# Kernel tuning notes

Measured on AMD Instinct MI355X. Metric: run time of the kernel, lower is better.

The kernel has to match this reference:

```python
import jax, jax.numpy as jnp
import numpy as np

B, LATENT = 8192, 1024
NR, NC = 12, 12                      # nb_rows, nb_cols
H0, W0 = NR + 2, NC + 2              # 14x14 after reshape
EPS = 1e-5
SLOPE = 0.01                         # LeakyReLU default


def setup_inputs() -> dict:
    key = jax.random.key(0)
    ks = jax.random.split(key, 9)
    s = 0.05
    return {
        "x": jax.random.normal(ks[0], (B, LATENT), jnp.float32),
        "fc_w": jax.random.normal(ks[1], (H0 * W0 * 36, LATENT), jnp.float32) * s,
        "fc_b": jax.random.normal(ks[2], (H0 * W0 * 36,), jnp.float32) * s,
        "conv_w": jax.random.normal(ks[3], (16, 36, 2, 2), jnp.float32) * s,
        "conv_b": jax.random.normal(ks[4], (16,), jnp.float32) * s,
        "gamma": jnp.ones((16,), jnp.float32),
        "beta": jnp.zeros((16,), jnp.float32),
        # locally-connected weights: (out_ch, in_ch, Hout, Wout, k*k)
        "lw1": jax.random.normal(ks[5], (6, 16, H0 - 1, W0 - 1, 4), jnp.float32) * s,
        "lw2": jax.random.normal(ks[6], (1, 6, H0 - 2, W0 - 2, 4), jnp.float32) * s,
    }


def _leaky(x):
    return jnp.where(x >= 0, x, SLOPE * x)


def _local_conv2(x, w):
    # x: (B,C,H,W); w: (O,C,Ho,Wo,4) with k=2, stride 1, no padding
    Ho, Wo = w.shape[2], w.shape[3]
    patches = jnp.stack(
        [x[:, :, dy:dy + Ho, dx:dx + Wo] for dy in (0, 1) for dx in (0, 1)],
        axis=-1)  # (B,C,Ho,Wo,4)
    return jnp.einsum('bchwk,ochwk->bohw', patches, w)


def reference(x, fc_w, fc_b, conv_w, conv_b, gamma, beta, lw1, lw2):
    # fc -> view(B, H0, W0, 36) -> permute to NCHW
    h = x @ fc_w.T + fc_b
    h = h.reshape(B, H0, W0, 36).transpose(0, 3, 1, 2)  # (B,36,14,14)
    # Conv2d k=2 padding='same' (torch pads bottom/right for even kernels)
    h = jax.lax.conv_general_dilated(
        h, conv_w, window_strides=(1, 1), padding=((0, 1), (0, 1)),
        dimension_numbers=('NCHW', 'OIHW', 'NCHW')) + conv_b[None, :, None, None]
    h = _leaky(h)
    # BatchNorm2d (training mode: batch stats, biased var)
    mu = h.mean(axis=(0, 2, 3), keepdims=True)
    var = h.var(axis=(0, 2, 3), keepdims=True)
    h = (h - mu) * jax.lax.rsqrt(var + EPS)
    h = h * gamma[None, :, None, None] + beta[None, :, None, None]
    # locally-connected stack: 14x14 -> 13x13 -> 12x12
    h = _leaky(_local_conv2(h, lw1))
    return _local_conv2(h, lw2)  # (B,1,12,12)
```

## Files before the change

kernel.cpp:

```cpp
#include <hip/hip_runtime.h>


#define SLOPE 0.01f

typedef __bf16 bf16x8 __attribute__((ext_vector_type(8)));
typedef float f32x4 __attribute__((ext_vector_type(4)));

typedef const __attribute__((address_space(1))) void* gas_ptr;
typedef __attribute__((address_space(3))) void* las_ptr;

__device__ __forceinline__ void load16_to_lds(const void* g, void* l) {
  __builtin_amdgcn_global_load_lds((gas_ptr)g, (las_ptr)l, 16, 0, 0);
}

__device__ __forceinline__ unsigned short f2bf(float f) {
  union { float f; unsigned int u; } v; v.f = f;
  unsigned int r = v.u + 0x7FFFu + ((v.u >> 16) & 1u);
  return (unsigned short)(r >> 16);
}
__device__ __forceinline__ float bfbits2f(unsigned int bits16) {
  union { unsigned int u; float f; } v; v.u = bits16 << 16;
  return v.f;
}
__device__ __forceinline__ float leaky(float v) { return v >= 0.f ? v : SLOPE * v; }

__global__ void k_cast_x(const float* __restrict__ x, unsigned short* __restrict__ xb,
                         float* __restrict__ stats) {
  if (blockIdx.x == 0 && threadIdx.x < 32) stats[threadIdx.x] = 0.f;
  int gid = blockIdx.x * 256 + threadIdx.x;
  const float4* x4 = (const float4*)x;
  float4 a = x4[gid * 2], b = x4[gid * 2 + 1];
  union { unsigned short s[8]; uint4 v; } o;
  o.s[0] = f2bf(a.x); o.s[1] = f2bf(a.y); o.s[2] = f2bf(a.z); o.s[3] = f2bf(a.w);
  o.s[4] = f2bf(b.x); o.s[5] = f2bf(b.y); o.s[6] = f2bf(b.z); o.s[7] = f2bf(b.w);
  ((uint4*)xb)[gid] = o.v;
}

__global__ void k_fold(const float* __restrict__ fc_w, const float* __restrict__ fc_b,
                       const float* __restrict__ conv_w, const float* __restrict__ conv_b,
                       unsigned short* __restrict__ Wc, float* __restrict__ bc) {
  __shared__ float cw[2304];
  int blk = blockIdx.x, t = threadIdx.x;
  if (blk == 196) {
    uint4 z = make_uint4(0, 0, 0, 0);
    uint4* dst = (uint4*)(Wc + 3136 * 1024);
    for (int i = t; i < 8192; i += 256) dst[i] = z;
    for (int i = 3136 + t; i < 3200; i += 256) bc[i] = 0.f;
    return;
  }
  for (int i = t; i < 2304; i += 256) cw[i] = conv_w[i];
  __syncthreads();
  int i0 = blk / 14, j0 = blk - (blk / 14) * 14;
  float acc[16][4];
#pragma unroll
  for (int o = 0; o < 16; o++)
#pragma unroll
    for (int q = 0; q < 4; q++) acc[o][q] = 0.f;
  for (int c = 0; c < 36; c++) {
#pragma unroll
    for (int dy = 0; dy < 2; dy++) {
      int ii = i0 + dy; if (ii > 13) continue;
#pragma unroll
      for (int dx = 0; dx < 2; dx++) {
        int jj = j0 + dx; if (jj > 13) continue;
        int row = (ii * 14 + jj) * 36 + c;
        float4 f = *(const float4*)(fc_w + row * 1024 + t * 4);
        int kk = dy * 2 + dx;
#pragma unroll
        for (int o = 0; o < 16; o++) {
          float w = cw[(o * 36 + c) * 4 + kk];
          acc[o][0] += w * f.x; acc[o][1] += w * f.y;
          acc[o][2] += w * f.z; acc[o][3] += w * f.w;
        }
      }
    }
  }
#pragma unroll
  for (int o = 0; o < 16; o++) {
    int n = o * 196 + i0 * 14 + j0;
    union { unsigned short s[4]; uint2 v; } u;
    u.s[0] = f2bf(acc[o][0]); u.s[1] = f2bf(acc[o][1]);
    u.s[2] = f2bf(acc[o][2]); u.s[3] = f2bf(acc[o][3]);
    *(uint2*)(Wc + n * 1024 + t * 4) = u.v;
  }
  if (t < 16) {
    int o = t;
    float b = conv_b[o];
    for (int c = 0; c < 36; c++)
      for (int dy = 0; dy < 2; dy++) {
        int ii = i0 + dy; if (ii > 13) continue;
        for (int dx = 0; dx < 2; dx++) {
          int jj = j0 + dx; if (jj > 13) continue;
          b += cw[(o * 36 + c) * 4 + dy * 2 + dx] * fc_b[(ii * 14 + jj) * 36 + c];
        }
      }
    bc[o * 196 + i0 * 14 + j0] = b;
  }
}

__global__ __launch_bounds__(256, 2) void k_gemm(const unsigned short* __restrict__ Xb,
                                                 const unsigned short* __restrict__ Wcb,
                                                 const float* __restrict__ bc,
                                                 unsigned short* __restrict__ h2) {
  __shared__ __align__(16) char lds[16384];
  const int t = threadIdx.x;
  const int w = t >> 6, lane = t & 63;
  const int quad = lane >> 4, l15 = lane & 15;
  const int m0 = blockIdx.y * 128, n0 = blockIdx.x * 128;
  const int mrow = t & 127, tko = t >> 7;
  const unsigned short* ga = Xb + (m0 + mrow) * 1024 + tko * 8;
  const unsigned short* gb = Wcb + (n0 + mrow) * 1024 + tko * 8;
  char* lA = lds;
  char* lB = lds + 8192;
  const int wbase = w * 1024;
  const int wm0 = (w >> 1) * 64, wn0 = (w & 1) * 64;

  f32x4 acc[4][4];
#pragma unroll
  for (int a = 0; a < 4; a++)
#pragma unroll
    for (int b = 0; b < 4; b++) acc[a][b] = (f32x4){0.f, 0.f, 0.f, 0.f};

  for (int kb = 0; kb < 1024; kb += 32) {
    __syncthreads();
    load16_to_lds(ga + kb,      lA + wbase);
    load16_to_lds(ga + kb + 16, lA + 4096 + wbase);
    load16_to_lds(gb + kb,      lB + wbase);
    load16_to_lds(gb + kb + 16, lB + 4096 + wbase);
    __syncthreads();

    bf16x8 af[4], bfr[4];
#pragma unroll
    for (int mb = 0; mb < 4; mb++)
      af[mb] = *(const bf16x8*)(lA + quad * 2048 + (wm0 + mb * 16 + l15) * 16);
#pragma unroll
    for (int nb = 0; nb < 4; nb++)
      bfr[nb] = *(const bf16x8*)(lB + quad * 2048 + (wn0 + nb * 16 + l15) * 16);
#pragma unroll
    for (int mb = 0; mb < 4; mb++)
#pragma unroll
      for (int nb = 0; nb < 4; nb++)
        acc[mb][nb] = __builtin_amdgcn_mfma_f32_16x16x32_bf16(af[mb], bfr[nb], acc[mb][nb], 0, 0, 0);
  }

#pragma unroll
  for (int nb = 0; nb < 4; nb++) {
    int col = n0 + wn0 + nb * 16 + l15;
    float bias = bc[col];
#pragma unroll
    for (int mb = 0; mb < 4; mb++) {
#pragma unroll
      for (int r = 0; r < 4; r++) {
        int row = m0 + wm0 + mb * 16 + quad * 4 + r;
        float v = acc[mb][nb][r] + bias;
        h2[row * 3200 + col] = f2bf(leaky(v));
      }
    }
  }
}

__global__ void k_stats(const unsigned short* __restrict__ h2, float* __restrict__ stats) {
  int o = blockIdx.x;
  int b0 = blockIdx.y * 64;
  float s = 0.f, s2 = 0.f;
  for (int i = threadIdx.x; i < 64 * 98; i += 256) {
    int b = i / 98, q = i - b * 98;
    unsigned int u = *(const unsigned int*)(h2 + (b0 + b) * 3200 + o * 196 + q * 2);
    float v0 = bfbits2f(u & 0xffffu), v1 = bfbits2f(u >> 16);
    s += v0 + v1; s2 += v0 * v0 + v1 * v1;
  }
  for (int off = 32; off; off >>= 1) {
    s += __shfl_down(s, off, 64);
    s2 += __shfl_down(s2, off, 64);
  }
  __shared__ float ps[8];
  int wv = threadIdx.x >> 6, lane = threadIdx.x & 63;
  if (lane == 0) { ps[wv * 2] = s; ps[wv * 2 + 1] = s2; }
  __syncthreads();
  if (threadIdx.x == 0) {
    atomicAdd(&stats[o],      ps[0] + ps[2] + ps[4] + ps[6]);
    atomicAdd(&stats[16 + o], ps[1] + ps[3] + ps[5] + ps[7]);
  }
}

__global__ __launch_bounds__(256) void k_tail(const unsigned short* __restrict__ h2,
                                              const float* __restrict__ stats,
                                              const float* __restrict__ gamma,
                                              const float* __restrict__ beta,
                                              const float* __restrict__ lw1,
                                              const float* __restrict__ lw2,
                                              float* __restrict__ out) {
  __shared__ unsigned short h3[4 * 3138];
  __shared__ float h4[4 * 1015];
  __shared__ float sc[16], sh[16];
  int b0 = blockIdx.x * 4, t = threadIdx.x;
  if (t < 16) {
    const float inv = 1.f / 1605632.f;
    float mean = stats[t] * inv;
    float var = stats[16 + t] * inv - mean * mean;
    float rstd = rsqrtf(var + 1e-5f);
    float s = gamma[t] * rstd;
    sc[t] = s; sh[t] = beta[t] - mean * s;
  }
  __syncthreads();
  for (int i = t; i < 6272; i += 256) {
    int bb = i / 1568, q = i - bb * 1568;
    int n = q * 2, o = n / 196;
    unsigned int u = *(const unsigned int*)(h2 + (b0 + bb) * 3200 + n);
    float v0 = bfbits2f(u & 0xffffu) * sc[o] + sh[o];
    float v1 = bfbits2f(u >> 16) * sc[o] + sh[o];
    unsigned int pk = (unsigned int)f2bf(v0) | ((unsigned int)f2bf(v1) << 16);
    *(unsigned int*)(h3 + bb * 3138 + n) = pk;
  }
  __syncthreads();
  for (int u = t; u < 312; u += 256) {
    int bb = u & 3, rest = u >> 2;
    int o = rest / 13, y = rest - o * 13;
    float acc[13];
#pragma unroll
    for (int x = 0; x < 13; x++) acc[x] = 0.f;
    const unsigned short* hb = h3 + bb * 3138;
    for (int c = 0; c < 16; c++) {
      float r0[14], r1[14];
      const unsigned int* p0 = (const unsigned int*)(hb + c * 196 + y * 14);
      const unsigned int* p1 = (const unsigned int*)(hb + c * 196 + (y + 1) * 14);
#pragma unroll
      for (int q = 0; q < 7; q++) {
        unsigned int v0 = p0[q], v1 = p1[q];
        r0[2 * q] = bfbits2f(v0 & 0xffffu); r0[2 * q + 1] = bfbits2f(v0 >> 16);
        r1[2 * q] = bfbits2f(v1 & 0xffffu); r1[2 * q + 1] = bfbits2f(v1 >> 16);
      }
      const float* wp = lw1 + (((o * 16 + c) * 13 + y) * 13) * 4;
#pragma unroll
      for (int x = 0; x < 13; x++)
        acc[x] += r0[x] * wp[x * 4] + r0[x + 1] * wp[x * 4 + 1] +
                  r1[x] * wp[x * 4 + 2] + r1[x + 1] * wp[x * 4 + 3];
    }
#pragma unroll
    for (int x = 0; x < 13; x++)
      h4[bb * 1015 + (o * 13 + y) * 13 + x] = leaky(acc[x]);
  }
  __syncthreads();
  for (int oi = t; oi < 576; oi += 256) {
    int pos = oi >> 2, bb = oi & 3;
    int y = pos / 12, x = pos - y * 12;
    float a = 0.f;
    const float* hp = h4 + bb * 1015;
#pragma unroll
    for (int c = 0; c < 6; c++) {
      const float* wpc = lw2 + ((c * 12 + y) * 12 + x) * 4;
      int hb = c * 169 + y * 13 + x;
      a += hp[hb] * wpc[0] + hp[hb + 1] * wpc[1] +
           hp[hb + 13] * wpc[2] + hp[hb + 14] * wpc[3];
    }
    out[(b0 + bb) * 144 + pos] = a;
  }
}

extern "C" void kernel_launch(void* const* d_in, const int* in_sizes, int n_in,
                              void* d_out, int out_size, void* d_ws, size_t ws_size,
                              hipStream_t stream) {
  const float* x      = (const float*)d_in[0];
  const float* fc_w   = (const float*)d_in[1];
  const float* fc_b   = (const float*)d_in[2];
  const float* conv_w = (const float*)d_in[3];
  const float* conv_b = (const float*)d_in[4];
  const float* gamma  = (const float*)d_in[5];
  const float* beta   = (const float*)d_in[6];
  const float* lw1    = (const float*)d_in[7];
  const float* lw2    = (const float*)d_in[8];

  char* ws = (char*)d_ws;
  unsigned short* Xb    = (unsigned short*)(ws);
  unsigned short* Wc    = (unsigned short*)(ws + 16777216);
  float*          bc    = (float*)(ws + 23330816);
  float*          stats = (float*)(ws + 23343616);
  unsigned short* h2    = (unsigned short*)(ws + 23343744);

  k_cast_x<<<4096, 256, 0, stream>>>(x, Xb, stats);
  k_fold<<<197, 256, 0, stream>>>(fc_w, fc_b, conv_w, conv_b, Wc, bc);
  k_gemm<<<dim3(25, 64), 256, 0, stream>>>(Xb, Wc, bc, h2);
  k_stats<<<dim3(16, 128), 256, 0, stream>>>(h2, stats);
  k_tail<<<2048, 256, 0, stream>>>(h2, stats, gamma, beta, lw1, lw2, (float*)d_out);
}
```

Baseline: 427.9 us.

## Transpose GEMM output, fuse BN stats into epilogue, split tail into batch-parallel kernels

The GEMM now writes h2 column-major (feature-major, batch contiguous) and accumulates per-column sum and sum-of-squares in its epilogue with atomics, which removes the separate stats pass over h2. A tiny kernel reduces the column stats to per-channel BN scale and shift. The tail is split into two kernels where each thread handles one batch element, giving coalesced loads across the batch, and h4 is stored in bf16. The fold kernel is spread across 4x more blocks, and the GEMM grid is relinearised so consecutive blocks share the same weight tile. The risks are extra atomics in the GEMM epilogue, one more launch, and large per-thread register arrays in tail1.

New measurement: 444.3 us. 1.04x slower.

```diff
diff --git a/kernel.cpp b/kernel.cpp
--- a/kernel.cpp
+++ b/kernel.cpp
@@ -25,8 +25,9 @@
 __device__ __forceinline__ float leaky(float v) { return v >= 0.f ? v : SLOPE * v; }
 
 __global__ void k_cast_x(const float* __restrict__ x, unsigned short* __restrict__ xb,
-                         float* __restrict__ stats) {
-  if (blockIdx.x == 0 && threadIdx.x < 32) stats[threadIdx.x] = 0.f;
+                         float* __restrict__ stats_col) {
+  if (blockIdx.x == 0)
+    for (int i = threadIdx.x; i < 6400; i += 256) stats_col[i] = 0.f;
   int gid = blockIdx.x * 256 + threadIdx.x;
   const float4* x4 = (const float4*)x;
   float4 a = x4[gid * 2], b = x4[gid * 2 + 1];
@@ -39,23 +40,24 @@
 __global__ void k_fold(const float* __restrict__ fc_w, const float* __restrict__ fc_b,
                        const float* __restrict__ conv_w, const float* __restrict__ conv_b,
                        unsigned short* __restrict__ Wc, float* __restrict__ bc) {
-  __shared__ float cw[2304];
-  int blk = blockIdx.x, t = threadIdx.x;
+  int blk = blockIdx.y, kq = blockIdx.x, t = threadIdx.x;
   if (blk == 196) {
     uint4 z = make_uint4(0, 0, 0, 0);
-    uint4* dst = (uint4*)(Wc + 3136 * 1024);
-    for (int i = t; i < 8192; i += 256) dst[i] = z;
-    for (int i = 3136 + t; i < 3200; i += 256) bc[i] = 0.f;
+    for (int i = t; i < 64 * 64; i += 256) {
+      int r = i >> 6, qq = i & 63;
+      *(uint4*)(Wc + (3136 + r) * 1024 + kq * 256 + qq * 8) = z;
+    }
+    if (kq == 0) for (int i = 3136 + t; i < 3200; i += 256) bc[i] = 0.f;
     return;
   }
+  __shared__ float cw[2304];
   for (int i = t; i < 2304; i += 256) cw[i] = conv_w[i];
   __syncthreads();
   int i0 = blk / 14, j0 = blk - (blk / 14) * 14;
-  float acc[16][4];
-#pragma unroll
-  for (int o = 0; o < 16; o++)
-#pragma unroll
-    for (int q = 0; q < 4; q++) acc[o][q] = 0.f;
+  int k = kq * 256 + t;
+  float acc[16];
+#pragma unroll
+  for (int o = 0; o < 16; o++) acc[o] = 0.f;
   for (int c = 0; c < 36; c++) {
 #pragma unroll
     for (int dy = 0; dy < 2; dy++) {
@@ -63,27 +65,17 @@
 #pragma unroll
       for (int dx = 0; dx < 2; dx++) {
         int jj = j0 + dx; if (jj > 13) continue;
-        int row = (ii * 14 + jj) * 36 + c;
-        float4 f = *(const float4*)(fc_w + row * 1024 + t * 4);
+        float f = fc_w[((ii * 14 + jj) * 36 + c) * 1024 + k];
         int kk = dy * 2 + dx;
 #pragma unroll
-        for (int o = 0; o < 16; o++) {
-          float w = cw[(o * 36 + c) * 4 + kk];
-          acc[o][0] += w * f.x; acc[o][1] += w * f.y;
-          acc[o][2] += w * f.z; acc[o][3] += w * f.w;
-        }
+        for (int o = 0; o < 16; o++) acc[o] += cw[(o * 36 + c) * 4 + kk] * f;
       }
     }
   }
 #pragma unroll
-  for (int o = 0; o < 16; o++) {
-    int n = o * 196 + i0 * 14 + j0;
-    union { unsigned short s[4]; uint2 v; } u;
-    u.s[0] = f2bf(acc[o][0]); u.s[1] = f2bf(acc[o][1]);
-    u.s[2] = f2bf(acc[o][2]); u.s[3] = f2bf(acc[o][3]);
-    *(uint2*)(Wc + n * 1024 + t * 4) = u.v;
-  }
-  if (t < 16) {
+  for (int o = 0; o < 16; o++)
+    Wc[(o * 196 + i0 * 14 + j0) * 1024 + k] = f2bf(acc[o]);
+  if (kq == 0 && t < 16) {
     int o = t;
     float b = conv_b[o];
     for (int c = 0; c < 36; c++)
@@ -101,12 +93,14 @@
 __global__ __launch_bounds__(256, 2) void k_gemm(const unsigned short* __restrict__ Xb,
                                                  const unsigned short* __restrict__ Wcb,
                                                  const float* __restrict__ bc,
-                                                 unsigned short* __restrict__ h2) {
+                                                 unsigned short* __restrict__ h2,
+                                                 float* __restrict__ stats_col) {
   __shared__ __align__(16) char lds[16384];
   const int t = threadIdx.x;
   const int w = t >> 6, lane = t & 63;
   const int quad = lane >> 4, l15 = lane & 15;
-  const int m0 = blockIdx.y * 128, n0 = blockIdx.x * 128;
+  const int lid = blockIdx.x;
+  const int m0 = (lid & 63) * 128, n0 = (lid >> 6) * 128;
   const int mrow = t & 127, tko = t >> 7;
   const unsigned short* ga = Xb + (m0 + mrow) * 1024 + tko * 8;
   const unsigned short* gb = Wcb + (n0 + mrow) * 1024 + tko * 8;
@@ -147,114 +141,114 @@
   for (int nb = 0; nb < 4; nb++) {
     int col = n0 + wn0 + nb * 16 + l15;
     float bias = bc[col];
+    float s = 0.f, s2 = 0.f;
+    unsigned short* base = h2 + col * 8192 + m0 + wm0 + quad * 4;
 #pragma unroll
     for (int mb = 0; mb < 4; mb++) {
+      union { unsigned short u[4]; uint2 v; } pk;
 #pragma unroll
       for (int r = 0; r < 4; r++) {
-        int row = m0 + wm0 + mb * 16 + quad * 4 + r;
-        float v = acc[mb][nb][r] + bias;
-        h2[row * 3200 + col] = f2bf(leaky(v));
+        float v = leaky(acc[mb][nb][r] + bias);
+        s += v; s2 += v * v;
+        pk.u[r] = f2bf(v);
       }
-    }
-  }
-}
-
-__global__ void k_stats(const unsigned short* __restrict__ h2, float* __restrict__ stats) {
-  int o = blockIdx.x;
-  int b0 = blockIdx.y * 64;
-  float s = 0.f, s2 = 0.f;
-  for (int i = threadIdx.x; i < 64 * 98; i += 256) {
-    int b = i / 98, q = i - b * 98;
-    unsigned int u = *(const unsigned int*)(h2 + (b0 + b) * 3200 + o * 196 + q * 2);
-    float v0 = bfbits2f(u & 0xffffu), v1 = bfbits2f(u >> 16);
-    s += v0 + v1; s2 += v0 * v0 + v1 * v1;
-  }
-  for (int off = 32; off; off >>= 1) {
-    s += __shfl_down(s, off, 64);
-    s2 += __shfl_down(s2, off, 64);
-  }
-  __shared__ float ps[8];
-  int wv = threadIdx.x >> 6, lane = threadIdx.x & 63;
-  if (lane == 0) { ps[wv * 2] = s; ps[wv * 2 + 1] = s2; }
+      *(uint2*)(base + mb * 16) = pk.v;
+    }
+    s  += __shfl_xor(s, 16, 64);  s  += __shfl_xor(s, 32, 64);
+    s2 += __shfl_xor(s2, 16, 64); s2 += __shfl_xor(s2, 32, 64);
+    if (quad == 0) {
+      atomicAdd(&stats_col[col], s);
+      atomicAdd(&stats_col[3200 + col], s2);
+    }
+  }
+}
+
+__global__ void k_bnscale(const float* __restrict__ stats_col,
+                          const float* __restrict__ gamma, const float* __restrict__ beta,
+                          float* __restrict__ scbuf) {
+  __shared__ float chs[16], chs2[16];
+  int t = threadIdx.x;
+  if (t < 16) { chs[t] = 0.f; chs2[t] = 0.f; }
   __syncthreads();
-  if (threadIdx.x == 0) {
-    atomicAdd(&stats[o],      ps[0] + ps[2] + ps[4] + ps[6]);
-    atomicAdd(&stats[16 + o], ps[1] + ps[3] + ps[5] + ps[7]);
-  }
-}
-
-__global__ __launch_bounds__(256) void k_tail(const unsigned short* __restrict__ h2,
-                                              const float* __restrict__ stats,
-                                              const float* __restrict__ gamma,
-                                              const float* __restrict__ beta,
-                                              const float* __restrict__ lw1,
-                                              const float* __restrict__ lw2,
-                                              float* __restrict__ out) {
-  __shared__ unsigned short h3[4 * 3138];
-  __shared__ float h4[4 * 1015];
-  __shared__ float sc[16], sh[16];
-  int b0 = blockIdx.x * 4, t = threadIdx.x;
+  for (int col = t; col < 3136; col += 256) {
+    int o = col / 196;
+    atomicAdd(&chs[o], stats_col[col]);
+    atomicAdd(&chs2[o], stats_col[3200 + col]);
+  }
+  __syncthreads();
   if (t < 16) {
     const float inv = 1.f / 1605632.f;
-    float mean = stats[t] * inv;
-    float var = stats[16 + t] * inv - mean * mean;
-    float rstd = rsqrtf(var + 1e-5f);
-    float s = gamma[t] * rstd;
-    sc[t] = s; sh[t] = beta[t] - mean * s;
-  }
-  __syncthreads();
-  for (int i = t; i < 6272; i += 256) {
-    int bb = i / 1568, q = i - bb * 1568;
-    int n = q * 2, o = n / 196;
-    unsigned int u = *(const unsigned int*)(h2 + (b0 + bb) * 3200 + n);
-    float v0 = bfbits2f(u & 0xffffu) * sc[o] + sh[o];
-    float v1 = bfbits2f(u >> 16) * sc[o] + sh[o];
-    unsigned int pk = (unsigned int)f2bf(v0) | ((unsigned int)f2bf(v1) << 16);
-    *(unsigned int*)(h3 + bb * 3138 + n) = pk;
-  }
-  __syncthreads();
-  for (int u = t; u < 312; u += 256) {
-    int bb = u & 3, rest = u >> 2;
-    int o = rest / 13, y = rest - o * 13;
-    float acc[13];
-#pragma unroll
-    for (int x = 0; x < 13; x++) acc[x] = 0.f;
-    const unsigned short* hb = h3 + bb * 3138;
-    for (int c = 0; c < 16; c++) {
-      float r0[14], r1[14];
-      const unsigned int* p0 = (const unsigned int*)(hb + c * 196 + y * 14);
-      const unsigned int* p1 = (const unsigned int*)(hb + c * 196 + (y + 1) * 14);
-#pragma unroll
-      for (int q = 0; q < 7; q++) {
-        unsigned int v0 = p0[q], v1 = p1[q];
-        r0[2 * q] = bfbits2f(v0 & 0xffffu); r0[2 * q + 1] = bfbits2f(v0 >> 16);
-        r1[2 * q] = bfbits2f(v1 & 0xffffu); r1[2 * q + 1] = bfbits2f(v1 >> 16);
-      }
+    float mean = chs[t] * inv;
+    float var = chs2[t] * inv - mean * mean;
+    float sc = gamma[t] * rsqrtf(var + 1e-5f);
+    scbuf[t] = sc; scbuf[16 + t] = beta[t] - mean * sc;
+  }
+}
+
+__global__ __launch_bounds__(64) void k_tail1(const unsigned short* __restrict__ h2,
+                                              const float* __restrict__ scbuf,
+                                              const float* __restrict__ lw1,
+                                              unsigned short* __restrict__ h4) {
+  const int m = blockIdx.x * 64 + threadIdx.x;
+  const int y = blockIdx.y;
+  float acc[6][13];
+#pragma unroll
+  for (int o = 0; o < 6; o++)
+#pragma unroll
+    for (int x = 0; x < 13; x++) acc[o][x] = 0.f;
+
+  for (int c = 0; c < 16; c++) {
+    float scc = scbuf[c], shc = scbuf[16 + c];
+    const unsigned short* p0 = h2 + (c * 196 + y * 14) * 8192 + m;
+    float r0[14], r1[14];
+#pragma unroll
+    for (int x = 0; x < 14; x++) {
+      r0[x] = bfbits2f(p0[x * 8192]) * scc + shc;
+      r1[x] = bfbits2f(p0[(14 + x) * 8192]) * scc + shc;
+    }
+#pragma unroll
+    for (int o = 0; o < 6; o++) {
       const float* wp = lw1 + (((o * 16 + c) * 13 + y) * 13) * 4;
 #pragma unroll
       for (int x = 0; x < 13; x++)
-        acc[x] += r0[x] * wp[x * 4] + r0[x + 1] * wp[x * 4 + 1] +
-                  r1[x] * wp[x * 4 + 2] + r1[x + 1] * wp[x * 4 + 3];
-    }
+        acc[o][x] += r0[x] * wp[4 * x] + r0[x + 1] * wp[4 * x + 1] +
+                     r1[x] * wp[4 * x + 2] + r1[x + 1] * wp[4 * x + 3];
+    }
+  }
+  unsigned short* q = h4 + y * 13 * 8192 + m;
+#pragma unroll
+  for (int o = 0; o < 6; o++)
 #pragma unroll
     for (int x = 0; x < 13; x++)
-      h4[bb * 1015 + (o * 13 + y) * 13 + x] = leaky(acc[x]);
-  }
-  __syncthreads();
-  for (int oi = t; oi < 576; oi += 256) {
-    int pos = oi >> 2, bb = oi & 3;
-    int y = pos / 12, x = pos - y * 12;
-    float a = 0.f;
-    const float* hp = h4 + bb * 1015;
-#pragma unroll
-    for (int c = 0; c < 6; c++) {
-      const float* wpc = lw2 + ((c * 12 + y) * 12 + x) * 4;
-      int hb = c * 169 + y * 13 + x;
-      a += hp[hb] * wpc[0] + hp[hb + 1] * wpc[1] +
-           hp[hb + 13] * wpc[2] + hp[hb + 14] * wpc[3];
-    }
-    out[(b0 + bb) * 144 + pos] = a;
-  }
+      q[(o * 169 + x) * 8192] = f2bf(leaky(acc[o][x]));
+}
+
+__global__ __launch_bounds__(256) void k_tail2(const unsigned short* __restrict__ h4,
+                                               const float* __restrict__ lw2,
+                                               float* __restrict__ out) {
+  const int lane = threadIdx.x & 63, w = threadIdx.x >> 6;
+  const int m = blockIdx.x * 64 + lane;
+  const int y = blockIdx.y * 4 + w;
+  float acc[12];
+#pragma unroll
+  for (int x = 0; x < 12; x++) acc[x] = 0.f;
+  for (int c = 0; c < 6; c++) {
+    const unsigned short* p = h4 + (c * 13 + y) * 13 * 8192 + m;
+    float r0[13], r1[13];
+#pragma unroll
+    for (int x = 0; x < 13; x++) {
+      r0[x] = bfbits2f(p[x * 8192]);
+      r1[x] = bfbits2f(p[(13 + x) * 8192]);
+    }
+    const float* wp = lw2 + ((c * 12 + y) * 12) * 4;
+#pragma unroll
+    for (int x = 0; x < 12; x++)
+      acc[x] += r0[x] * wp[4 * x] + r0[x + 1] * wp[4 * x + 1] +
+                r1[x] * wp[4 * x + 2] + r1[x + 1] * wp[4 * x + 3];
+  }
+  float* op = out + m * 144 + y * 12;
+#pragma unroll
+  for (int x = 0; x < 12; x++) op[x] = acc[x];
 }
 
 extern "C" void kernel_launch(void* const* d_in, const int* in_sizes, int n_in,
@@ -271,15 +265,18 @@
   const float* lw2    = (const float*)d_in[8];
 
   char* ws = (char*)d_ws;
-  unsigned short* Xb    = (unsigned short*)(ws);
-  unsigned short* Wc    = (unsigned short*)(ws + 16777216);
-  float*          bc    = (float*)(ws + 23330816);
-  float*          stats = (float*)(ws + 23343616);
-  unsigned short* h2    = (unsigned short*)(ws + 23343744);
-
-  k_cast_x<<<4096, 256, 0, stream>>>(x, Xb, stats);
-  k_fold<<<197, 256, 0, stream>>>(fc_w, fc_b, conv_w, conv_b, Wc, bc);
-  k_gemm<<<dim3(25, 64), 256, 0, stream>>>(Xb, Wc, bc, h2);
-  k_stats<<<dim3(16, 128), 256, 0, stream>>>(h2, stats);
-  k_tail<<<2048, 256, 0, stream>>>(h2, stats, gamma, beta, lw1, lw2, (float*)d_out);
-}
+  unsigned short* Xb        = (unsigned short*)(ws);
+  unsigned short* h4T       = (unsigned short*)(ws);
+  unsigned short* Wc        = (unsigned short*)(ws + 16777216);
+  float*          bc        = (float*)(ws + 23330816);
+  float*          stats_col = (float*)(ws + 23343616);
+  float*          scbuf     = (float*)(ws + 23369216);
+  unsigned short* h2T       = (unsigned short*)(ws + 23369344);
+
+  k_cast_x<<<4096, 256, 0, stream>>>(x, Xb, stats_col);
+  k_fold<<<dim3(4, 197), 256, 0, stream>>>(fc_w, fc_b, conv_w, conv_b, Wc, bc);
+  k_gemm<<<1600, 256, 0, stream>>>(Xb, Wc, bc, h2T, stats_col);
+  k_bnscale<<<1, 256, 0, stream>>>(stats_col, gamma, beta, scbuf);
+  k_tail1<<<dim3(128, 13), 64, 0, stream>>>(h2T, scbuf, lw1, h4T);
+  k_tail2<<<dim3(128, 3), 256, 0, stream>>>(h4T, lw2, (float*)d_out);
+}
```
